# Optimization experiments

Measured on AMD Instinct MI355X. Metric: run time of the kernel, lower is better.

## Reference

```python
import jax, jax.numpy as jnp
import numpy as np


def setup_inputs() -> dict:
    key = jax.random.key(0)
    k1, k2, k3, k4 = jax.random.split(key, 4)
    B, N, M, D = 4, 8192, 8192, 3
    pred = jax.random.normal(k1, (B, N, D), dtype=jnp.float32)
    target = jax.random.normal(k2, (B, M, D), dtype=jnp.float32)
    bpp = jax.random.uniform(k3, (), dtype=jnp.float32)
    lamda = jax.random.uniform(k4, (), dtype=jnp.float32)
    return {"pred": pred, "target": target, "bpp": bpp, "lamda": lamda}


def _chamfer(pred, target):
    # pred: [B, N, 3], target: [B, M, 3]
    # squared pairwise distances: [B, N, M]
    diff = pred[:, :, None, :] - target[:, None, :, :]
    d2 = jnp.sum(diff * diff, axis=-1)
    cham_x = jnp.min(d2, axis=2).mean(axis=1)  # [B] pred -> target
    cham_y = jnp.min(d2, axis=1).mean(axis=1)  # [B] target -> pred
    return (cham_x + cham_y).mean()  # batch-mean of summed directions (pytorch3d default)


def reference(pred, target, bpp, lamda):
    dist = _chamfer(pred, target)
    return dist + lamda * bpp
```

## Files before the change

### kernel.cpp

```cpp
#include <hip/hip_runtime.h>

#define NPTS 8192
#define NB 4

#define WPB 4
#define ITILES 8
#define ROWS_PER_WAVE (ITILES * 16)
#define ROWS_PER_BLOCK (WPB * ROWS_PER_WAVE)
#define CHUNK 512
#define JT (CHUNK / 16)
#define CHUNKS (NPTS / CHUNK)
#define ROWBLKS (NPTS / ROWS_PER_BLOCK)

using bf16x8 = __attribute__((ext_vector_type(8))) short;
using f32x4  = __attribute__((ext_vector_type(4))) float;

__device__ __forceinline__ unsigned short bfb(float v) {
    unsigned int x = __float_as_uint(v);
    return (unsigned short)((x + 0x7FFFu + ((x >> 16) & 1u)) >> 16);
}
__device__ __forceinline__ float bff(unsigned short u) {
    return __uint_as_float(((unsigned int)u) << 16);
}
__device__ __forceinline__ void split3(float v, unsigned short& H,
                                       unsigned short& M, unsigned short& L) {
    H = bfb(v); float r = v - bff(H);
    M = bfb(r); L = bfb(r - bff(M));
}
__device__ __forceinline__ unsigned int pk(unsigned short lo, unsigned short hi) {
    return (unsigned int)lo | ((unsigned int)hi << 16);
}
__device__ __forceinline__ unsigned int umn(unsigned int a, unsigned int b) {
    return a < b ? a : b;
}

__device__ __forceinline__ void tile_pair(
    const bf16x8 (&af)[ITILES], bf16x8 b0, bf16x8 b1,
    f32x4 (&rmin)[ITILES], unsigned int* colh, int colw, int lane,
    const f32x4& zf)
{
    f32x4 cp0 = {3e38f, 3e38f, 3e38f, 3e38f};
    f32x4 cp1 = {3e38f, 3e38f, 3e38f, 3e38f};
#pragma unroll
    for (int it = 0; it < ITILES; it += 2) {
        f32x4 d00 = __builtin_amdgcn_mfma_f32_16x16x32_bf16(af[it],     b0, zf, 0, 0, 0);
        f32x4 d01 = __builtin_amdgcn_mfma_f32_16x16x32_bf16(af[it],     b1, zf, 0, 0, 0);
        f32x4 d10 = __builtin_amdgcn_mfma_f32_16x16x32_bf16(af[it + 1], b0, zf, 0, 0, 0);
        f32x4 d11 = __builtin_amdgcn_mfma_f32_16x16x32_bf16(af[it + 1], b1, zf, 0, 0, 0);
#pragma unroll
        for (int r = 0; r < 4; ++r) {
            rmin[it][r]     = fminf(fminf(d00[r], d01[r]), rmin[it][r]);
            rmin[it + 1][r] = fminf(fminf(d10[r], d11[r]), rmin[it + 1][r]);
            cp0[r]          = fminf(fminf(d00[r], d10[r]), cp0[r]);
            cp1[r]          = fminf(fminf(d01[r], d11[r]), cp1[r]);
        }
    }
    float c0 = fminf(fminf(cp0[0], cp0[1]), fminf(cp0[2], cp0[3]));
    float c1 = fminf(fminf(cp1[0], cp1[1]), fminf(cp1[2], cp1[3]));
    c0 = fmaxf(c0, 0.f);
    c1 = fmaxf(c1, 0.f);
    const int a = (lane >> 4) * CHUNK + colw + (lane & 15);
    atomicMin(&colh[a],      __float_as_uint(c0));
    atomicMin(&colh[a + 16], __float_as_uint(c1));
}

__global__ __launch_bounds__(256, 4) void chamfer_fused(
    const float* __restrict__ pred, const float* __restrict__ target,
    float* __restrict__ rowpart, float* __restrict__ colpart,
    float* __restrict__ out, const float* __restrict__ bpp,
    const float* __restrict__ lamda)
{
    __shared__ short bB[JT * 512];
    __shared__ unsigned int colh[4 * CHUNK];

    const int tid  = threadIdx.x;
    const int lane = tid & 63;
    const int w    = tid >> 6;
    const int bid  = blockIdx.x;
    const int ck   = bid & (CHUNKS - 1);
    const int rb   = (bid >> 4) & (ROWBLKS - 1);
    const int b    = bid >> 8;

    if (bid == 0 && tid == 0) out[0] = lamda[0] * bpp[0];

    for (int i = tid; i < 4 * CHUNK; i += 256) colh[i] = 0x7F7F7F7Fu;

    const int col0 = ck * CHUNK;
    const float* asrc = pred   + (size_t)b * NPTS * 3;
    const float* bsrc = target + (size_t)b * NPTS * 3;
    const unsigned short ONE = 0x3F80u;

    for (int i = tid; i < ROWS_PER_BLOCK; i += 256) {
        int g = rb * ROWS_PER_BLOCK + i;
        float x = asrc[3 * g + 0], y = asrc[3 * g + 1], z = asrc[3 * g + 2];
        float pp = fmaf(x, x, fmaf(y, y, z * z));
        unsigned short xH,xM,xL, yH,yM,yL, zH,zM,zL, pH,pM,pL;
        split3(-2.f * x, xH, xM, xL);
        split3(-2.f * y, yH, yM, yL);
        split3(-2.f * z, zH, zM, zL);
        split3(pp, pH, pM, pL);
        uint4 q0 = make_uint4(pk(xH,xH), pk(xM,xH), pk(xL,xM), pk(yH,yH));
        uint4 q1 = make_uint4(pk(yM,yH), pk(yL,yM), pk(zH,zH), pk(zM,zH));
        uint4 q2 = make_uint4(pk(zL,zM), pk(pH,pM), pk(pL,ONE), pk(ONE,ONE));
        uint4 q3 = make_uint4(0u, 0u, 0u, 0u);
        char* base = (char*)bB + (i >> 7) * 8192 + ((i & 127) >> 4) * 1024 + (i & 15) * 16;
        *(uint4*)(base +   0) = q0;
        *(uint4*)(base + 256) = q1;
        *(uint4*)(base + 512) = q2;
        *(uint4*)(base + 768) = q3;
    }
    __syncthreads();

    bf16x8 af[ITILES];
    {
        const char* ab = (const char*)bB + w * 8192 + lane * 16;
#pragma unroll
        for (int it = 0; it < ITILES; ++it)
            af[it] = *(const bf16x8*)(ab + it * 1024);
    }
    __syncthreads();

    for (int pc = tid; pc < CHUNK; pc += 256) {
        int g = col0 + pc;
        float x = bsrc[3 * g + 0], y = bsrc[3 * g + 1], z = bsrc[3 * g + 2];
        float pp = fmaf(x, x, fmaf(y, y, z * z));
        unsigned short xH,xM,xL, yH,yM,yL, zH,zM,zL, pH,pM,pL;
        split3(x, xH, xM, xL);
        split3(y, yH, yM, yL);
        split3(z, zH, zM, zL);
        split3(pp, pH, pM, pL);
        uint4 q0 = make_uint4(pk(xH,xM), pk(xH,xL), pk(xH,xM), pk(yH,yM));
        uint4 q1 = make_uint4(pk(yH,yL), pk(yH,yM), pk(zH,zM), pk(zH,zL));
        uint4 q2 = make_uint4(pk(zH,zM), pk(ONE,ONE), pk(ONE,pH), pk(pM,pL));
        char* base = (char*)bB + (pc >> 4) * 1024 + (pc & 15) * 16;
        *(uint4*)(base +   0) = q0;
        *(uint4*)(base + 256) = q1;
        *(uint4*)(base + 512) = q2;
    }

    f32x4 rmin[ITILES];
#pragma unroll
    for (int it = 0; it < ITILES; ++it) {
        rmin[it][0] = 3e38f; rmin[it][1] = 3e38f;
        rmin[it][2] = 3e38f; rmin[it][3] = 3e38f;
    }
    const f32x4 zf = {0.f, 0.f, 0.f, 0.f};

    __syncthreads();

    const char* bb = (const char*)bB + lane * 16;
    bf16x8 B0 = *(const bf16x8*)(bb);
    bf16x8 B1 = *(const bf16x8*)(bb + 1024);
    int colw = 0;
    for (int jt = 0; jt < JT; jt += 2) {
        int nj = (jt + 2) & (JT - 1);
        bf16x8 Bn0 = *(const bf16x8*)(bb + nj * 1024);
        bf16x8 Bn1 = *(const bf16x8*)(bb + (nj + 1) * 1024);
        tile_pair(af, B0, B1, rmin, colh, colw, lane, zf);
        colw += 32;
        B0 = Bn0; B1 = Bn1;
    }

#pragma unroll
    for (int it = 0; it < ITILES; ++it) {
#pragma unroll
        for (int r = 0; r < 4; ++r) {
            float v = rmin[it][r];
            v = fminf(v, __shfl_xor(v, 1, 64));
            v = fminf(v, __shfl_xor(v, 2, 64));
            v = fminf(v, __shfl_xor(v, 4, 64));
            v = fminf(v, __shfl_xor(v, 8, 64));
            if ((lane & 15) == 0) {
                int row = rb * ROWS_PER_BLOCK + w * ROWS_PER_WAVE
                        + it * 16 + (lane >> 4) * 4 + r;
                rowpart[((size_t)(b * CHUNKS) + ck) * NPTS + row] = fmaxf(v, 0.f);
            }
        }
    }

    __syncthreads();
    for (int i = tid; i < CHUNK; i += 256) {
        unsigned int m = umn(umn(colh[i],            colh[CHUNK + i]),
                             umn(colh[2 * CHUNK + i], colh[3 * CHUNK + i]));
        colpart[((size_t)(b * ROWBLKS) + rb) * NPTS + col0 + i] = __uint_as_float(m);
    }
}

__global__ __launch_bounds__(256) void reduce_partials(
    const float* __restrict__ rowpart, const float* __restrict__ colpart,
    float* __restrict__ out)
{
    const int tid = threadIdx.x;
    const int gt  = blockIdx.x * 256 + tid;
    float s = 0.f;
#pragma unroll
    for (int a = 0; a < 2; a++) {
        const float* P = a ? colpart : rowpart;
#pragma unroll
        for (int cc = 0; cc < 2; cc++) {
            int c = gt + cc * 16384;
            int b = c >> 13, r = c & 8191;
            const float* p = P + (size_t)b * 16 * NPTS + r;
            float m = p[0];
#pragma unroll
            for (int k = 1; k < 16; k++)
                m = fminf(m, p[(size_t)k * NPTS]);
            s += m;
        }
    }
#pragma unroll
    for (int off = 32; off > 0; off >>= 1) s += __shfl_down(s, off, 64);
    __shared__ float red[4];
    int lane = tid & 63, wid = tid >> 6;
    if (lane == 0) red[wid] = s;
    __syncthreads();
    if (tid == 0)
        atomicAdd(out, (red[0] + red[1] + red[2] + red[3]) * (1.0f / 32768.0f));
}

#define T 256
#define Q 8
#define S 16
#define CH 512
#define NCOMBO 8

__global__ __launch_bounds__(T) void chamfer_partial(
    const float* __restrict__ pred, const float* __restrict__ target,
    unsigned int* __restrict__ partmin)
{
    __shared__ float4 db[CH + 2];

    const int bid   = blockIdx.x;
    const int dbc   = bid & (S - 1);
    const int qc    = (bid >> 4) & 3;
    const int combo = bid >> 6;
    const int dir   = combo & 1;
    const int b     = combo >> 1;

    const float* qptr = (dir == 0 ? pred : target) + (size_t)b * NPTS * 3;
    const float* dptr = (dir == 0 ? target : pred) + (size_t)b * NPTS * 3;

    const int tid = threadIdx.x;

    for (int p = tid; p < CH; p += T) {
        int gj = dbc * CH + p;
        float x = dptr[gj * 3 + 0];
        float y = dptr[gj * 3 + 1];
        float z = dptr[gj * 3 + 2];
        db[p] = make_float4(-2.f * x, -2.f * y, -2.f * z,
                            x * x + y * y + z * z);
    }

    float qx[Q], qy[Q], qz[Q], m[Q];
    int qi0 = qc * (T * Q) + tid;
#pragma unroll
    for (int k = 0; k < Q; k++) {
        int qi = qi0 + k * T;
        qx[k] = qptr[qi * 3 + 0];
        qy[k] = qptr[qi * 3 + 1];
        qz[k] = qptr[qi * 3 + 2];
        m[k]  = 3.4e38f;
    }
    __syncthreads();

    float4 c0 = db[0], c1 = db[1];
    for (int j = 0; j < CH; j += 2) {
        float4 n0 = db[j + 2];
        float4 n1 = db[j + 3];
#pragma unroll
        for (int k = 0; k < Q; k++) {
            float s0 = fmaf(c0.x, qx[k], fmaf(c0.y, qy[k], fmaf(c0.z, qz[k], c0.w)));
            float s1 = fmaf(c1.x, qx[k], fmaf(c1.y, qy[k], fmaf(c1.z, qz[k], c1.w)));
            m[k] = fminf(m[k], fminf(s0, s1));
        }
        c0 = n0; c1 = n1;
    }

#pragma unroll
    for (int k = 0; k < Q; k++) {
        int qi = qi0 + k * T;
        float qq = fmaf(qx[k], qx[k], fmaf(qy[k], qy[k], qz[k] * qz[k]));
        float d2 = fmaxf(m[k] + qq, 0.0f);
        atomicMin(&partmin[combo * NPTS + qi], __float_as_uint(d2));
    }
}

__global__ __launch_bounds__(1024) void reduce_final(
    const unsigned int* __restrict__ partmin,
    const float* __restrict__ bpp, const float* __restrict__ lamda,
    float* __restrict__ out)
{
    const int tid = threadIdx.x;
    float s = 0.f;
#pragma unroll
    for (int k = 0; k < (NCOMBO * NPTS) / 1024; k++)
        s += __uint_as_float(partmin[tid + k * 1024]);

#pragma unroll
    for (int off = 32; off > 0; off >>= 1)
        s += __shfl_down(s, off, 64);

    __shared__ float red[16];
    int lane = tid & 63, wid = tid >> 6;
    if (lane == 0) red[wid] = s;
    __syncthreads();
    if (wid == 0) {
        s = (lane < 16) ? red[lane] : 0.f;
#pragma unroll
        for (int off = 8; off > 0; off >>= 1)
            s += __shfl_down(s, off, 64);
        if (lane == 0)
            out[0] = s * (1.0f / 32768.0f) + lamda[0] * bpp[0];
    }
}

extern "C" void kernel_launch(void* const* d_in, const int* in_sizes, int n_in,
                              void* d_out, int out_size, void* d_ws, size_t ws_size,
                              hipStream_t stream) {
    const float* pred   = (const float*)d_in[0];
    const float* target = (const float*)d_in[1];
    const float* bpp    = (const float*)d_in[2];
    const float* lamda  = (const float*)d_in[3];

    const size_t part_bytes = (size_t)NB * 16 * NPTS * sizeof(float);

    if (ws_size >= 2 * part_bytes) {
        float* rowpart = (float*)d_ws;
        float* colpart = rowpart + (size_t)NB * 16 * NPTS;
        chamfer_fused<<<NB * ROWBLKS * CHUNKS, 256, 0, stream>>>(
            pred, target, rowpart, colpart, (float*)d_out, bpp, lamda);
        reduce_partials<<<64, 256, 0, stream>>>(rowpart, colpart, (float*)d_out);
    } else {
        unsigned int* partmin = (unsigned int*)d_ws;
        hipMemsetAsync(partmin, 0x7F, (size_t)NCOMBO * NPTS * sizeof(unsigned int),
                       stream);
        chamfer_partial<<<NCOMBO * 4 * S, T, 0, stream>>>(pred, target, partmin);
        reduce_final<<<1, 1024, 0, stream>>>(partmin, bpp, lamda, (float*)d_out);
    }
}
```

Before: 85.27 us.

## Interleave column-min LDS layout, hoist point loads, drop a block barrier

The column-min scratch in LDS becomes interleaved (column*4 + quad), so each wave's atomicMin calls hit 64 consecutive words instead of four groups 512 words apart, which should avoid bank conflicts. The final per-column reduction then reads all four partials with one 128-bit LDS load. Global loads of pred and target points are issued up front, before LDS initialisation, so their latency overlaps that setup. Each wave now encodes only the A rows it reads itself, which removes one block-wide __syncthreads. This relies on LDS ordering within a single wave.

Result: no change. 85.06 us (-0.2%).

```diff
diff --git a/kernel.cpp b/kernel.cpp
--- a/kernel.cpp
+++ b/kernel.cpp
@@ -34,9 +34,42 @@
     return a < b ? a : b;
 }
 
+__device__ __forceinline__ void encA(float x, float y, float z, char* base) {
+    const unsigned short ONE = 0x3F80u;
+    float pp = fmaf(x, x, fmaf(y, y, z * z));
+    unsigned short xH,xM,xL, yH,yM,yL, zH,zM,zL, pH,pM,pL;
+    split3(-2.f * x, xH, xM, xL);
+    split3(-2.f * y, yH, yM, yL);
+    split3(-2.f * z, zH, zM, zL);
+    split3(pp, pH, pM, pL);
+    uint4 q0 = make_uint4(pk(xH,xH), pk(xM,xH), pk(xL,xM), pk(yH,yH));
+    uint4 q1 = make_uint4(pk(yM,yH), pk(yL,yM), pk(zH,zH), pk(zM,zH));
+    uint4 q2 = make_uint4(pk(zL,zM), pk(pH,pM), pk(pL,ONE), pk(ONE,ONE));
+    uint4 q3 = make_uint4(0u, 0u, 0u, 0u);
+    *(uint4*)(base +   0) = q0;
+    *(uint4*)(base + 256) = q1;
+    *(uint4*)(base + 512) = q2;
+    *(uint4*)(base + 768) = q3;
+}
+__device__ __forceinline__ void encB(float x, float y, float z, char* base) {
+    const unsigned short ONE = 0x3F80u;
+    float pp = fmaf(x, x, fmaf(y, y, z * z));
+    unsigned short xH,xM,xL, yH,yM,yL, zH,zM,zL, pH,pM,pL;
+    split3(x, xH, xM, xL);
+    split3(y, yH, yM, yL);
+    split3(z, zH, zM, zL);
+    split3(pp, pH, pM, pL);
+    uint4 q0 = make_uint4(pk(xH,xM), pk(xH,xL), pk(xH,xM), pk(yH,yM));
+    uint4 q1 = make_uint4(pk(yH,yL), pk(yH,yM), pk(zH,zM), pk(zH,zL));
+    uint4 q2 = make_uint4(pk(zH,zM), pk(ONE,ONE), pk(ONE,pH), pk(pM,pL));
+    *(uint4*)(base +   0) = q0;
+    *(uint4*)(base + 256) = q1;
+    *(uint4*)(base + 512) = q2;
+}
+
 __device__ __forceinline__ void tile_pair(
     const bf16x8 (&af)[ITILES], bf16x8 b0, bf16x8 b1,
-    f32x4 (&rmin)[ITILES], unsigned int* colh, int colw, int lane,
+    f32x4 (&rmin)[ITILES], unsigned int* colh, int cbase,
     const f32x4& zf)
 {
     f32x4 cp0 = {3e38f, 3e38f, 3e38f, 3e38f};
@@ -59,9 +92,8 @@
     float c1 = fminf(fminf(cp1[0], cp1[1]), fminf(cp1[2], cp1[3]));
     c0 = fmaxf(c0, 0.f);
     c1 = fmaxf(c1, 0.f);
-    const int a = (lane >> 4) * CHUNK + colw + (lane & 15);
-    atomicMin(&colh[a],      __float_as_uint(c0));
-    atomicMin(&colh[a + 16], __float_as_uint(c1));
+    atomicMin(&colh[cbase],      __float_as_uint(c0));
+    atomicMin(&colh[cbase + 64], __float_as_uint(c1));
 }
 
 __global__ __launch_bounds__(256, 4) void chamfer_fused(
@@ -71,7 +103,7 @@
     const float* __restrict__ lamda)
 {
     __shared__ short bB[JT * 512];
-    __shared__ unsigned int colh[4 * CHUNK];
+    __shared__ unsigned int colh[CHUNK * 4];
 
     const int tid  = threadIdx.x;
     const int lane = tid & 63;
@@ -81,35 +113,28 @@
     const int rb   = (bid >> 4) & (ROWBLKS - 1);
     const int b    = bid >> 8;
 
-    if (bid == 0 && tid == 0) out[0] = lamda[0] * bpp[0];
-
-    for (int i = tid; i < 4 * CHUNK; i += 256) colh[i] = 0x7F7F7F7Fu;
-
     const int col0 = ck * CHUNK;
     const float* asrc = pred   + (size_t)b * NPTS * 3;
     const float* bsrc = target + (size_t)b * NPTS * 3;
-    const unsigned short ONE = 0x3F80u;
-
-    for (int i = tid; i < ROWS_PER_BLOCK; i += 256) {
-        int g = rb * ROWS_PER_BLOCK + i;
-        float x = asrc[3 * g + 0], y = asrc[3 * g + 1], z = asrc[3 * g + 2];
-        float pp = fmaf(x, x, fmaf(y, y, z * z));
-        unsigned short xH,xM,xL, yH,yM,yL, zH,zM,zL, pH,pM,pL;
-        split3(-2.f * x, xH, xM, xL);
-        split3(-2.f * y, yH, yM, yL);
-        split3(-2.f * z, zH, zM, zL);
-        split3(pp, pH, pM, pL);
-        uint4 q0 = make_uint4(pk(xH,xH), pk(xM,xH), pk(xL,xM), pk(yH,yH));
-        uint4 q1 = make_uint4(pk(yM,yH), pk(yL,yM), pk(zH,zH), pk(zM,zH));
-        uint4 q2 = make_uint4(pk(zL,zM), pk(pH,pM), pk(pL,ONE), pk(ONE,ONE));
-        uint4 q3 = make_uint4(0u, 0u, 0u, 0u);
-        char* base = (char*)bB + (i >> 7) * 8192 + ((i & 127) >> 4) * 1024 + (i & 15) * 16;
-        *(uint4*)(base +   0) = q0;
-        *(uint4*)(base + 256) = q1;
-        *(uint4*)(base + 512) = q2;
-        *(uint4*)(base + 768) = q3;
-    }
-    __syncthreads();
+
+    const int ag0 = rb * ROWS_PER_BLOCK + w * ROWS_PER_WAVE + lane;
+    const int ag1 = ag0 + 64;
+    float a0x = asrc[3 * ag0 + 0], a0y = asrc[3 * ag0 + 1], a0z = asrc[3 * ag0 + 2];
+    float a1x = asrc[3 * ag1 + 0], a1y = asrc[3 * ag1 + 1], a1z = asrc[3 * ag1 + 2];
+    const int bg0 = col0 + tid;
+    const int bg1 = bg0 + 256;
+    float b0x = bsrc[3 * bg0 + 0], b0y = bsrc[3 * bg0 + 1], b0z = bsrc[3 * bg0 + 2];
+    float b1x = bsrc[3 * bg1 + 0], b1y = bsrc[3 * bg1 + 1], b1z = bsrc[3 * bg1 + 2];
+
+    if (bid == 0 && tid == 0) out[0] = lamda[0] * bpp[0];
+
+    for (int i = tid; i < CHUNK * 4; i += 256) colh[i] = 0x7F7F7F7Fu;
+
+    {
+        char* wbase = (char*)bB + w * 8192 + (lane & 15) * 16;
+        encA(a0x, a0y, a0z, wbase + (lane >> 4) * 1024);
+        encA(a1x, a1y, a1z, wbase + (4 + (lane >> 4)) * 1024);
+    }
 
     bf16x8 af[ITILES];
     {
@@ -120,23 +145,8 @@
     }
     __syncthreads();
 
-    for (int pc = tid; pc < CHUNK; pc += 256) {
-        int g = col0 + pc;
-        float x = bsrc[3 * g + 0], y = bsrc[3 * g + 1], z = bsrc[3 * g + 2];
-        float pp = fmaf(x, x, fmaf(y, y, z * z));
-        unsigned short xH,xM,xL, yH,yM,yL, zH,zM,zL, pH,pM,pL;
-        split3(x, xH, xM, xL);
-        split3(y, yH, yM, yL);
-        split3(z, zH, zM, zL);
-        split3(pp, pH, pM, pL);
-        uint4 q0 = make_uint4(pk(xH,xM), pk(xH,xL), pk(xH,xM), pk(yH,yM));
-        uint4 q1 = make_uint4(pk(yH,yL), pk(yH,yM), pk(zH,zM), pk(zH,zL));
-        uint4 q2 = make_uint4(pk(zH,zM), pk(ONE,ONE), pk(ONE,pH), pk(pM,pL));
-        char* base = (char*)bB + (pc >> 4) * 1024 + (pc & 15) * 16;
-        *(uint4*)(base +   0) = q0;
-        *(uint4*)(base + 256) = q1;
-        *(uint4*)(base + 512) = q2;
-    }
+    encB(b0x, b0y, b0z, (char*)bB + (bg0 - col0 >> 4) * 1024 + ((bg0 - col0) & 15) * 16);
+    encB(b1x, b1y, b1z, (char*)bB + (bg1 - col0 >> 4) * 1024 + ((bg1 - col0) & 15) * 16);
 
     f32x4 rmin[ITILES];
 #pragma unroll
@@ -151,13 +161,13 @@
     const char* bb = (const char*)bB + lane * 16;
     bf16x8 B0 = *(const bf16x8*)(bb);
     bf16x8 B1 = *(const bf16x8*)(bb + 1024);
-    int colw = 0;
+    int cbase = (lane & 15) * 4 + (lane >> 4);
     for (int jt = 0; jt < JT; jt += 2) {
         int nj = (jt + 2) & (JT - 1);
         bf16x8 Bn0 = *(const bf16x8*)(bb + nj * 1024);
         bf16x8 Bn1 = *(const bf16x8*)(bb + (nj + 1) * 1024);
-        tile_pair(af, B0, B1, rmin, colh, colw, lane, zf);
-        colw += 32;
+        tile_pair(af, B0, B1, rmin, colh, cbase, zf);
+        cbase += 128;
         B0 = Bn0; B1 = Bn1;
     }
 
@@ -180,8 +190,8 @@
 
     __syncthreads();
     for (int i = tid; i < CHUNK; i += 256) {
-        unsigned int m = umn(umn(colh[i],            colh[CHUNK + i]),
-                             umn(colh[2 * CHUNK + i], colh[3 * CHUNK + i]));
+        uint4 v = *(const uint4*)&colh[i * 4];
+        unsigned int m = umn(umn(v.x, v.y), umn(v.z, v.w));
         colpart[((size_t)(b * ROWBLKS) + rb) * NPTS + col0 + i] = __uint_as_float(m);
     }
 }
```
